# Kernel optimization log

Measured on AMD Instinct MI355X. Metric: run time of the kernel, lower is better.

Reference implementation:

```python
import jax, jax.numpy as jnp
import numpy as np

NHEADS = 16
HEAD_DIM = 64
HIDDEN = 1024
QKV = NHEADS * HEAD_DIM  # 1024
SCALING = HEAD_DIM ** -0.5


def setup_inputs() -> dict:
    key = jax.random.key(0)
    k1, k2, k3, k4, k5 = jax.random.split(key, 5)
    B, S = 2, 2048
    hidden_states = jax.random.normal(k1, (B, S, HIDDEN), dtype=jnp.float32)
    # nn.Linear weights: stored [out, in]; kaiming-uniform-ish init scale
    w_qkv = jax.random.normal(k2, (3 * QKV, HIDDEN), dtype=jnp.float32) * (HIDDEN ** -0.5)
    b_qkv = jax.random.normal(k3, (3 * QKV,), dtype=jnp.float32) * 0.01
    w_o = jax.random.normal(k4, (HIDDEN, QKV), dtype=jnp.float32) * (QKV ** -0.5)
    b_o = jax.random.normal(k5, (HIDDEN,), dtype=jnp.float32) * 0.01
    return {"hidden_states": hidden_states, "w_qkv": w_qkv, "b_qkv": b_qkv,
            "w_o": w_o, "b_o": b_o}


def reference(hidden_states, w_qkv, b_qkv, w_o, b_o):
    B, S, _ = hidden_states.shape
    # qkv projection: x @ W^T + b  (torch nn.Linear convention)
    qkv = jnp.einsum('bsh,oh->bso', hidden_states, w_qkv) + b_qkv  # [B,S,3*QKV]
    xq, xk, xv = jnp.split(qkv, 3, axis=-1)
    # [B,S,H,D] -> [B,H,S,D]
    q = xq.reshape(B, S, NHEADS, HEAD_DIM).transpose(0, 2, 1, 3)
    k = xk.reshape(B, S, NHEADS, HEAD_DIM).transpose(0, 2, 1, 3)
    v = xv.reshape(B, S, NHEADS, HEAD_DIM).transpose(0, 2, 1, 3)
    scores = jnp.einsum('bhqd,bhkd->bhqk', q, k) * SCALING
    # dropout is identity in eval mode; mask is None in this config
    probs = jax.nn.softmax(scores.astype(jnp.float32), axis=-1).astype(q.dtype)
    out = jnp.einsum('bhqk,bhkd->bhqd', probs, v)  # [B,H,S,D]
    out = out.transpose(0, 2, 1, 3).reshape(B, S, QKV)
    return jnp.einsum('bsq,oq->bso', out, w_o) + b_o
```

## Files before the change

kernel.cpp:

```cpp
#include <hip/hip_runtime.h>

#define SEQ     2048
#define MROWS   4096
#define HID     1024
#define QKV3    3072
#define NH      16
#define HD      64
#define QSCALE  0.18033688f

typedef unsigned short u16;
typedef unsigned int   u32;
typedef __attribute__((ext_vector_type(8)))  short  bf16x8;
typedef __attribute__((ext_vector_type(4)))  float  floatx4;

__device__ __forceinline__ u16 f2bf(float f) {
    u32 u = __builtin_bit_cast(u32, f);
    u += 0x7fffu + ((u >> 16) & 1u);
    return (u16)(u >> 16);
}

#if __has_builtin(__builtin_amdgcn_cvt_pk_bf16_f32)
__device__ __forceinline__ ushort2 pack_bf(float a, float b) {
    auto r = __builtin_amdgcn_cvt_pk_bf16_f32(a, b);
    return __builtin_bit_cast(ushort2, r);
}
#else
__device__ __forceinline__ ushort2 pack_bf(float a, float b) {
    u32 ua = __builtin_bit_cast(u32, a) + 0x8000u;
    u32 ub = __builtin_bit_cast(u32, b) + 0x8000u;
    u32 d  = __builtin_amdgcn_perm(ub, ua, 0x07060302u);
    return __builtin_bit_cast(ushort2, d);
}
#endif

__device__ __forceinline__ void async_cp16(const void* g, void* l) {
    __builtin_amdgcn_global_load_lds(
        (const __attribute__((address_space(1))) unsigned int*)g,
        (__attribute__((address_space(3))) unsigned int*)l, 16, 0, 0);
}

#define N4_X   (MROWS * HID / 4)
#define N4_WQ  (QKV3 * HID / 4)
#define N4_WO  (HID * HID / 4)
__global__ void cvt_all(const float* __restrict__ x, const float* __restrict__ wq,
                        const float* __restrict__ wo, u16* __restrict__ xb,
                        u16* __restrict__ wqb, u16* __restrict__ wob) {
    int i = blockIdx.x * blockDim.x + threadIdx.x;
    const float* src; u16* dst; int k;
    if (i < N4_X)                { src = x;  dst = xb;  k = i; }
    else if (i < N4_X + N4_WQ)   { src = wq; dst = wqb; k = i - N4_X; }
    else                         { src = wo; dst = wob; k = i - N4_X - N4_WQ; }
    float4 v = ((const float4*)src)[k];
    ushort2 lo = pack_bf(v.x, v.y), hi = pack_bf(v.z, v.w);
    ushort4 o = {lo.x, lo.y, hi.x, hi.y};
    ((ushort4*)dst)[k] = o;
}

template <int MODE, int NT>
__global__ __launch_bounds__(256)
void gemm_bf16_nt(const u16* __restrict__ A, const u16* __restrict__ B,
                  const float* __restrict__ bias, float* __restrict__ Cout,
                  int M, int N, int K,
                  u16* __restrict__ q_ws, u16* __restrict__ k_ws,
                  u16* __restrict__ vt_ws) {
    constexpr int WN = NT / 2;
    constexpr int NJ = WN / 16;
    __shared__ u16 As[2][128 * 32];
    __shared__ u16 Bs[2][NT * 32];
    const int t  = (int)threadIdx.x;
    const int w  = t >> 6, l = t & 63;
    const int wr = w >> 1, wc = w & 1;
    const int m0 = (int)blockIdx.y * 128, n0 = (int)blockIdx.x * NT;
    const int lrow = l >> 2;
    const int lseg = ((l & 3) ^ ((l >> 3) & 3)) * 8;
    const int fm = l & 15, fq = l >> 4;
    const int fseg = (fq ^ ((fm >> 1) & 3)) * 8;

    auto stage = [&](int k0, int bb) {
#pragma unroll
        for (int rep = 0; rep < 2; ++rep) {
            const int chunk = w + rep * 4;
            const int row   = chunk * 16 + lrow;
            async_cp16(A + (size_t)(m0 + row) * K + k0 + lseg, &As[bb][chunk * 512]);
            if (NT == 128 || rep == 0)
                async_cp16(B + (size_t)(n0 + row) * K + k0 + lseg, &Bs[bb][chunk * 512]);
        }
    };

    floatx4 acc[4][NJ];
#pragma unroll
    for (int i = 0; i < 4; ++i)
#pragma unroll
        for (int j = 0; j < NJ; ++j) acc[i][j] = (floatx4)(0.f);

    const int T = K >> 5;
    stage(0, 0);
    for (int tt = 0; tt < T; ++tt) {
        const int cur = tt & 1;
        __syncthreads();
        if (tt + 1 < T) stage((tt + 1) << 5, cur ^ 1);
        bf16x8 af[4], bf[NJ];
#pragma unroll
        for (int i = 0; i < 4; ++i)
            af[i] = *(const bf16x8*)&As[cur][(wr * 64 + i * 16 + fm) * 32 + fseg];
#pragma unroll
        for (int j = 0; j < NJ; ++j)
            bf[j] = *(const bf16x8*)&Bs[cur][(wc * WN + j * 16 + fm) * 32 + fseg];
#pragma unroll
        for (int i = 0; i < 4; ++i)
#pragma unroll
            for (int j = 0; j < NJ; ++j)
                acc[i][j] = __builtin_amdgcn_mfma_f32_16x16x32_bf16(
                    af[i], bf[j], acc[i][j], 0, 0, 0);
    }

#pragma unroll
    for (int j = 0; j < NJ; ++j) {
        const int col = n0 + wc * WN + j * 16 + fm;
        const float bv = bias[col];
        const int region = col >> 10;
        const int hh = (col >> 6) & 15, d = col & 63;
#pragma unroll
        for (int i = 0; i < 4; ++i) {
            const int row0 = m0 + wr * 64 + i * 16 + fq * 4;
            if (MODE == 0) {
#pragma unroll
                for (int r = 0; r < 4; ++r)
                    Cout[(size_t)(row0 + r) * N + col] = acc[i][j][r] + bv;
            } else if (region < 2) {
                u16* __restrict__ dst = (region == 0) ? q_ws : k_ws;
                const float sc = (region == 0) ? QSCALE : 1.0f;
#pragma unroll
                for (int r = 0; r < 4; ++r) {
                    const int row = row0 + r;
                    const int b = row >> 11, s = row & 2047;
                    dst[((size_t)(b * NH + hh) * SEQ + s) * HD + d] =
                        f2bf((acc[i][j][r] + bv) * sc);
                }
            } else {
                const int b = row0 >> 11, s0 = row0 & 2047;
                ushort2 lo = pack_bf(acc[i][j][0] + bv, acc[i][j][1] + bv);
                ushort2 hi = pack_bf(acc[i][j][2] + bv, acc[i][j][3] + bv);
                ushort4 o = {lo.x, lo.y, hi.x, hi.y};
                *(ushort4*)&vt_ws[((size_t)(b * NH + hh) * HD + d) * SEQ + s0] = o;
            }
        }
    }
}

__global__ __launch_bounds__(512, 4)
void attn_mfma(const u16* __restrict__ qw, const u16* __restrict__ kw,
               const u16* __restrict__ vtw, u16* __restrict__ attn) {
    __shared__ u16 Ks [2][64 * 64];
    __shared__ u16 Vts[2][64 * 64];
    __shared__ u16 Ps[8][16 * 72];

    const int bh   = (int)blockIdx.x;
    const int qblk = (int)blockIdx.y * 128;
    const int t = (int)threadIdx.x;
    const int w = t >> 6, l = t & 63;
    const int fm = l & 15, fq = l >> 4;
    const int srow = l >> 3, sseg = l & 7;
    const size_t headSD = (size_t)bh * SEQ * HD;
    const size_t headDS = (size_t)bh * HD * SEQ;

    auto stage = [&](int kt, int bb) {
        async_cp16(kw + headSD + (size_t)(kt * 64 + w * 8 + srow) * HD
                       + ((sseg ^ srow) * 8), &Ks[bb][w * 512]);
        async_cp16(vtw + headDS + (size_t)(w * 8 + srow) * SEQ + kt * 64
                       + ((sseg ^ srow) * 8), &Vts[bb][w * 512]);
    };

    const int qrow = qblk + w * 16 + fm;
    bf16x8 qa[2];
#pragma unroll
    for (int kc = 0; kc < 2; ++kc)
        qa[kc] = *(const bf16x8*)(qw + headSD + (size_t)qrow * HD + kc * 32 + fq * 8);

    floatx4 oacc[4];
#pragma unroll
    for (int dt = 0; dt < 4; ++dt) oacc[dt] = (floatx4)(0.f);
    float psum = 0.f;

    stage(0, 0);
    for (int kt = 0; kt < SEQ / 64; ++kt) {
        const int cur = kt & 1;
        __syncthreads();
        if (kt + 1 < SEQ / 64) stage(kt + 1, cur ^ 1);

        floatx4 sacc[4];
#pragma unroll
        for (int j = 0; j < 4; ++j) sacc[j] = (floatx4)(0.f);
#pragma unroll
        for (int j = 0; j < 4; ++j) {
#pragma unroll
            for (int kc = 0; kc < 2; ++kc) {
                const int seg = (4 * kc + fq) ^ (fm & 7);
                bf16x8 ka = *(const bf16x8*)&Ks[cur][(j * 16 + fm) * 64 + seg * 8];
                sacc[j] = __builtin_amdgcn_mfma_f32_16x16x32_bf16(ka, qa[kc], sacc[j], 0, 0, 0);
            }
        }

#pragma unroll
        for (int j = 0; j < 4; ++j) {
            const float p0 = exp2f(sacc[j][0]);
            const float p1 = exp2f(sacc[j][1]);
            const float p2 = exp2f(sacc[j][2]);
            const float p3 = exp2f(sacc[j][3]);
            psum += (p0 + p1) + (p2 + p3);
            *(ushort2*)&Ps[w][fm * 72 + j * 16 + fq * 4]     = pack_bf(p0, p1);
            *(ushort2*)&Ps[w][fm * 72 + j * 16 + fq * 4 + 2] = pack_bf(p2, p3);
        }

#pragma unroll
        for (int kc = 0; kc < 2; ++kc) {
            bf16x8 pb = *(const bf16x8*)&Ps[w][fm * 72 + kc * 32 + fq * 8];
#pragma unroll
            for (int dt = 0; dt < 4; ++dt) {
                const int seg = (4 * kc + fq) ^ (fm & 7);
                bf16x8 va = *(const bf16x8*)&Vts[cur][(dt * 16 + fm) * 64 + seg * 8];
                oacc[dt] = __builtin_amdgcn_mfma_f32_16x16x32_bf16(va, pb, oacc[dt], 0, 0, 0);
            }
        }
    }

    psum += __shfl_xor(psum, 16);
    psum += __shfl_xor(psum, 32);
    const float inv = 1.0f / psum;

    const int b = bh >> 4, h = bh & 15;
    u16* __restrict__ orow =
        attn + (size_t)(b * SEQ + qblk + w * 16 + fm) * HID + h * HD;
#pragma unroll
    for (int dt = 0; dt < 4; ++dt) {
        *(ushort2*)&orow[dt * 16 + fq * 4]     = pack_bf(oacc[dt][0] * inv, oacc[dt][1] * inv);
        *(ushort2*)&orow[dt * 16 + fq * 4 + 2] = pack_bf(oacc[dt][2] * inv, oacc[dt][3] * inv);
    }
}

extern "C" void kernel_launch(void* const* d_in, const int* in_sizes, int n_in,
                              void* d_out, int out_size, void* d_ws, size_t ws_size,
                              hipStream_t stream) {
    const float* x     = (const float*)d_in[0];
    const float* w_qkv = (const float*)d_in[1];
    const float* b_qkv = (const float*)d_in[2];
    const float* w_o   = (const float*)d_in[3];
    const float* b_o   = (const float*)d_in[4];
    float* outp = (float*)d_out;

    u16* xb    = (u16*)d_ws;
    u16* wqkvb = xb    + (size_t)MROWS * HID;
    u16* wob   = wqkvb + (size_t)QKV3 * HID;
    u16* q_ws  = wob   + (size_t)HID * HID;
    u16* k_ws  = q_ws  + (size_t)MROWS * HID;
    u16* vt_ws = k_ws  + (size_t)MROWS * HID;
    u16* attnb = vt_ws + (size_t)MROWS * HID;

    const int blk = 256;
    cvt_all<<<(N4_X + N4_WQ + N4_WO) / blk, blk, 0, stream>>>(
        x, w_qkv, w_o, xb, wqkvb, wob);

    gemm_bf16_nt<1, 128><<<dim3(QKV3 / 128, MROWS / 128), blk, 0, stream>>>(
        xb, wqkvb, b_qkv, nullptr, MROWS, QKV3, HID, q_ws, k_ws, vt_ws);

    attn_mfma<<<dim3(NH * 2, SEQ / 128), 512, 0, stream>>>(q_ws, k_ws, vt_ws, attnb);

    gemm_bf16_nt<0, 64><<<dim3(HID / 64, MROWS / 128), blk, 0, stream>>>(
        attnb, wob, b_o, outp, MROWS, HID, HID, nullptr, nullptr, nullptr);
}
```

Baseline: 201.0 us.

## Load V fragments directly from global memory instead of staging through LDS

The attention kernel no longer stages V^T tiles into shared memory with async copies. Each lane now loads its V MFMA fragments straight from global memory into registers at the top of each key tile. This halves the LDS footprint and LDS read traffic per tile, but every one of the 8 waves re-reads the same V data from global or L2 with no sharing. Separately, the bf16 pack helper now returns a u32 so paired stores become single 64-bit writes.

```diff
diff --git a/kernel.cpp b/kernel.cpp
--- a/kernel.cpp
+++ b/kernel.cpp
@@ -20,16 +20,15 @@
 }
 
 #if __has_builtin(__builtin_amdgcn_cvt_pk_bf16_f32)
-__device__ __forceinline__ ushort2 pack_bf(float a, float b) {
+__device__ __forceinline__ u32 pack_bf(float a, float b) {
     auto r = __builtin_amdgcn_cvt_pk_bf16_f32(a, b);
-    return __builtin_bit_cast(ushort2, r);
+    return __builtin_bit_cast(u32, r);
 }
 #else
-__device__ __forceinline__ ushort2 pack_bf(float a, float b) {
+__device__ __forceinline__ u32 pack_bf(float a, float b) {
     u32 ua = __builtin_bit_cast(u32, a) + 0x8000u;
     u32 ub = __builtin_bit_cast(u32, b) + 0x8000u;
-    u32 d  = __builtin_amdgcn_perm(ub, ua, 0x07060302u);
-    return __builtin_bit_cast(ushort2, d);
+    return __builtin_amdgcn_perm(ub, ua, 0x07060302u);
 }
 #endif
 
@@ -51,9 +50,8 @@
     else if (i < N4_X + N4_WQ)   { src = wq; dst = wqb; k = i - N4_X; }
     else                         { src = wo; dst = wob; k = i - N4_X - N4_WQ; }
     float4 v = ((const float4*)src)[k];
-    ushort2 lo = pack_bf(v.x, v.y), hi = pack_bf(v.z, v.w);
-    ushort4 o = {lo.x, lo.y, hi.x, hi.y};
-    ((ushort4*)dst)[k] = o;
+    uint2 o = {pack_bf(v.x, v.y), pack_bf(v.z, v.w)};
+    ((uint2*)dst)[k] = o;
 }
 
 template <int MODE, int NT>
@@ -139,10 +137,9 @@
                 }
             } else {
                 const int b = row0 >> 11, s0 = row0 & 2047;
-                ushort2 lo = pack_bf(acc[i][j][0] + bv, acc[i][j][1] + bv);
-                ushort2 hi = pack_bf(acc[i][j][2] + bv, acc[i][j][3] + bv);
-                ushort4 o = {lo.x, lo.y, hi.x, hi.y};
-                *(ushort4*)&vt_ws[((size_t)(b * NH + hh) * HD + d) * SEQ + s0] = o;
+                uint2 o = {pack_bf(acc[i][j][0] + bv, acc[i][j][1] + bv),
+                           pack_bf(acc[i][j][2] + bv, acc[i][j][3] + bv)};
+                *(uint2*)&vt_ws[((size_t)(b * NH + hh) * HD + d) * SEQ + s0] = o;
             }
         }
     }
@@ -151,8 +148,7 @@
 __global__ __launch_bounds__(512, 4)
 void attn_mfma(const u16* __restrict__ qw, const u16* __restrict__ kw,
                const u16* __restrict__ vtw, u16* __restrict__ attn) {
-    __shared__ u16 Ks [2][64 * 64];
-    __shared__ u16 Vts[2][64 * 64];
+    __shared__ u16 Ks[2][64 * 64];
     __shared__ u16 Ps[8][16 * 72];
 
     const int bh   = (int)blockIdx.x;
@@ -164,11 +160,9 @@
     const size_t headSD = (size_t)bh * SEQ * HD;
     const size_t headDS = (size_t)bh * HD * SEQ;
 
-    auto stage = [&](int kt, int bb) {
+    auto stageK = [&](int kt, int bb) {
         async_cp16(kw + headSD + (size_t)(kt * 64 + w * 8 + srow) * HD
                        + ((sseg ^ srow) * 8), &Ks[bb][w * 512]);
-        async_cp16(vtw + headDS + (size_t)(w * 8 + srow) * SEQ + kt * 64
-                       + ((sseg ^ srow) * 8), &Vts[bb][w * 512]);
     };
 
     const int qrow = qblk + w * 16 + fm;
@@ -177,16 +171,26 @@
     for (int kc = 0; kc < 2; ++kc)
         qa[kc] = *(const bf16x8*)(qw + headSD + (size_t)qrow * HD + kc * 32 + fq * 8);
 
+    const u16* __restrict__ vbase = vtw + headDS + (size_t)fm * SEQ + fq * 8;
+
     floatx4 oacc[4];
 #pragma unroll
     for (int dt = 0; dt < 4; ++dt) oacc[dt] = (floatx4)(0.f);
     float psum = 0.f;
 
-    stage(0, 0);
+    stageK(0, 0);
     for (int kt = 0; kt < SEQ / 64; ++kt) {
         const int cur = kt & 1;
         __syncthreads();
-        if (kt + 1 < SEQ / 64) stage(kt + 1, cur ^ 1);
+        if (kt + 1 < SEQ / 64) stageK(kt + 1, cur ^ 1);
+
+        bf16x8 vf[2][4];
+#pragma unroll
+        for (int kc = 0; kc < 2; ++kc)
+#pragma unroll
+            for (int dt = 0; dt < 4; ++dt)
+                vf[kc][dt] = *(const bf16x8*)(vbase + (size_t)dt * 16 * SEQ
+                                              + kt * 64 + kc * 32);
 
         floatx4 sacc[4];
 #pragma unroll
@@ -208,19 +212,17 @@
             const float p2 = exp2f(sacc[j][2]);
             const float p3 = exp2f(sacc[j][3]);
             psum += (p0 + p1) + (p2 + p3);
-            *(ushort2*)&Ps[w][fm * 72 + j * 16 + fq * 4]     = pack_bf(p0, p1);
-            *(ushort2*)&Ps[w][fm * 72 + j * 16 + fq * 4 + 2] = pack_bf(p2, p3);
+            uint2 pk = {pack_bf(p0, p1), pack_bf(p2, p3)};
+            *(uint2*)&Ps[w][fm * 72 + j * 16 + fq * 4] = pk;
         }
 
 #pragma unroll
         for (int kc = 0; kc < 2; ++kc) {
             bf16x8 pb = *(const bf16x8*)&Ps[w][fm * 72 + kc * 32 + fq * 8];
 #pragma unroll
-            for (int dt = 0; dt < 4; ++dt) {
-                const int seg = (4 * kc + fq) ^ (fm & 7);
-                bf16x8 va = *(const bf16x8*)&Vts[cur][(dt * 16 + fm) * 64 + seg * 8];
-                oacc[dt] = __builtin_amdgcn_mfma_f32_16x16x32_bf16(va, pb, oacc[dt], 0, 0, 0);
-            }
+            for (int dt = 0; dt < 4; ++dt)
+                oacc[dt] = __builtin_amdgcn_mfma_f32_16x16x32_bf16(
+                    vf[kc][dt], pb, oacc[dt], 0, 0, 0);
         }
     }
 
@@ -233,8 +235,9 @@
         attn + (size_t)(b * SEQ + qblk + w * 16 + fm) * HID + h * HD;
 #pragma unroll
     for (int dt = 0; dt < 4; ++dt) {
-        *(ushort2*)&orow[dt * 16 + fq * 4]     = pack_bf(oacc[dt][0] * inv, oacc[dt][1] * inv);
-        *(ushort2*)&orow[dt * 16 + fq * 4 + 2] = pack_bf(oacc[dt][2] * inv, oacc[dt][3] * inv);
+        uint2 o = {pack_bf(oacc[dt][0] * inv, oacc[dt][1] * inv),
+                   pack_bf(oacc[dt][2] * inv, oacc[dt][3] * inv)};
+        *(uint2*)&orow[dt * 16 + fq * 4] = o;
     }
 }
 
```

Result: slower. 266.6 us (+32.6%).
